# Kernel tuning notes

Hardware: AMD Instinct MI355X
Metric: run time of the kernel (lower is better)

The kernel has to match this reference:

```python
import jax, jax.numpy as jnp
import numpy as np

B, T, D = 32, 512, 384
DUR_MAX = 8                 # durations drawn in [0, DUR_MAX)
MAX_OUT = T * (DUR_MAX - 1) # static upper bound on total expanded length (3584)
ALPHA = 1.0


def setup_inputs() -> dict:
    key = jax.random.key(0)
    k1, k2 = jax.random.split(key)
    x = jax.random.normal(k1, (B, T, D), dtype=jnp.float32)
    durations = jax.random.randint(k2, (B, T), 0, DUR_MAX, dtype=jnp.int32)
    return {"input": x, "durations": durations}


def reference(input, durations):
    # patched_dur = clamp(round(alpha * dur), min=0)
    patched = jnp.round(ALPHA * durations.astype(jnp.float32)).astype(jnp.int32)
    patched = jnp.maximum(patched, 0)                       # [B, T]
    cum = jnp.cumsum(patched, axis=1)                       # [B, T] exclusive-right boundaries
    total = cum[:, -1:]                                      # [B, 1] true expanded lengths

    pos = jnp.arange(MAX_OUT, dtype=jnp.int32)               # [MAX_OUT]
    # output frame j comes from token idx = first t with cum[t] > j
    idx = jax.vmap(lambda c: jnp.searchsorted(c, pos, side='right'))(cum)  # [B, MAX_OUT]
    idx = jnp.clip(idx, 0, T - 1)
    valid = pos[None, :] < total                              # [B, MAX_OUT]

    out = jnp.take_along_axis(input, idx[:, :, None], axis=1)  # [B, MAX_OUT, D]
    return jnp.where(valid[:, :, None], out, jnp.zeros((), dtype=input.dtype))
```

## Files before the change

kernel.cpp:

```cpp
#include <hip/hip_runtime.h>

#define NB 32
#define NT 512
#define ND 384
#define DUR_MAX 8
#define MAX_OUT (NT * (DUR_MAX - 1))
#define NV (ND / 4)
#define NWG ((NB * MAX_OUT * NV) / 256)

__global__ __launch_bounds__(NT) void lr_scan_scatter(
    const int* __restrict__ dur, int* __restrict__ idxmap)
{
    __shared__ int wsum[NT / 64];
    const int b    = blockIdx.x;
    const int t    = threadIdx.x;
    const int lane = t & 63;
    const int w    = t >> 6;

    int d = dur[b * NT + t];
    d = d > 0 ? d : 0;

    int v = d;
    #pragma unroll
    for (int off = 1; off < 64; off <<= 1) {
        int u = __shfl_up(v, off);
        if (lane >= off) v += u;
    }
    if (lane == 63) wsum[w] = v;
    __syncthreads();
    if (t == 0) {
        int acc = 0;
        #pragma unroll
        for (int i = 0; i < NT / 64; ++i) { acc += wsum[i]; wsum[i] = acc; }
    }
    __syncthreads();
    const int cum   = v + (w ? wsum[w - 1] : 0);
    const int total = wsum[NT / 64 - 1];
    const int start = cum - d;

    int* base = idxmap + b * MAX_OUT;
    const int src = (b * NT + t) * NV;
    for (int j = 0; j < d; ++j) base[start + j] = src;
    for (int s = total + t; s < MAX_OUT; s += NT) base[s] = -1;
}

__global__ __launch_bounds__(256) void lr_gather(
    const float4* __restrict__ in, const int* __restrict__ idxmap,
    float4* __restrict__ out)
{
    const unsigned bid = blockIdx.x;
    const unsigned per = NWG / 8;
    const unsigned swz = (bid & 7u) * per + (bid >> 3);
    const unsigned g   = swz * 256u + threadIdx.x;
    const unsigned row = g / NV;
    const unsigned col = g - row * NV;

    const int src = idxmap[row];
    float4 r = make_float4(0.f, 0.f, 0.f, 0.f);
    if (src >= 0) r = in[src + col];
    out[g] = r;
}

extern "C" void kernel_launch(void* const* d_in, const int* in_sizes, int n_in,
                              void* d_out, int out_size, void* d_ws, size_t ws_size,
                              hipStream_t stream)
{
    const float* x   = (const float*)d_in[0];
    const int*   dur = (const int*)d_in[1];
    float* out = (float*)d_out;

    int* idxmap = (int*)d_ws;

    lr_scan_scatter<<<NB, NT, 0, stream>>>(dur, idxmap);
    lr_gather<<<NWG, 256, 0, stream>>>((const float4*)x, idxmap, (float4*)out);
}
```

Measured before the change: 197.9 us.

## Fuse duration scan and gather into one kernel with per-window shared index map

Replaces the separate scan/scatter and gather kernels with one fused kernel. Each block recomputes the per-batch prefix sum over durations and builds a shared-memory index map for one of 16 output windows, then gathers rows straight into the output. This drops the global idxmap round trip and the second launch. In exchange every block redoes the 512-element scan and adds a barrier, and padded positions now issue a dummy load from row 0.

```diff
diff --git a/kernel.cpp b/kernel.cpp
--- a/kernel.cpp
+++ b/kernel.cpp
@@ -6,16 +6,29 @@
 #define DUR_MAX 8
 #define MAX_OUT (NT * (DUR_MAX - 1))
 #define NV (ND / 4)
-#define NWG ((NB * MAX_OUT * NV) / 256)
+#define NWIN 16
+#define WPOS (MAX_OUT / NWIN)
+#define NBLK (NB * NWIN)
+#define VPT (WPOS * NV / NT)
 
-__global__ __launch_bounds__(NT) void lr_scan_scatter(
-    const int* __restrict__ dur, int* __restrict__ idxmap)
+__global__ __launch_bounds__(NT) void lr_fused(
+    const int* __restrict__ dur, const float4* __restrict__ in,
+    float4* __restrict__ out)
 {
     __shared__ int wsum[NT / 64];
-    const int b    = blockIdx.x;
+    __shared__ int ridx[WPOS];
+
+    const unsigned bid = blockIdx.x;
+    const unsigned l   = (bid & 7u) * (NBLK / 8u) + (bid >> 3);
+    const int b  = (int)(l >> 4);
+    const int wb = (int)(l & 15u);
+    const int p0 = wb * WPOS;
+
     const int t    = threadIdx.x;
     const int lane = t & 63;
     const int w    = t >> 6;
+
+    if (t < WPOS) ridx[t] = -1;
 
     int d = dur[b * NT + t];
     d = d > 0 ? d : 0;
@@ -35,30 +48,26 @@
     }
     __syncthreads();
     const int cum   = v + (w ? wsum[w - 1] : 0);
-    const int total = wsum[NT / 64 - 1];
     const int start = cum - d;
 
-    int* base = idxmap + b * MAX_OUT;
+    int lo = start - p0;        if (lo < 0) lo = 0;
+    int hi = start + d - p0;    if (hi > WPOS) hi = WPOS;
     const int src = (b * NT + t) * NV;
-    for (int j = 0; j < d; ++j) base[start + j] = src;
-    for (int s = total + t; s < MAX_OUT; s += NT) base[s] = -1;
-}
+    for (int j = lo; j < hi; ++j) ridx[j] = src;
+    __syncthreads();
 
-__global__ __launch_bounds__(256) void lr_gather(
-    const float4* __restrict__ in, const int* __restrict__ idxmap,
-    float4* __restrict__ out)
-{
-    const unsigned bid = blockIdx.x;
-    const unsigned per = NWG / 8;
-    const unsigned swz = (bid & 7u) * per + (bid >> 3);
-    const unsigned g   = swz * 256u + threadIdx.x;
-    const unsigned row = g / NV;
-    const unsigned col = g - row * NV;
-
-    const int src = idxmap[row];
-    float4 r = make_float4(0.f, 0.f, 0.f, 0.f);
-    if (src >= 0) r = in[src + col];
-    out[g] = r;
+    float4* ob = out + ((size_t)b * MAX_OUT + p0) * NV;
+    for (int i = 0; i < VPT; ++i) {
+        const int g = i * NT + t;
+        const int r = g / NV;
+        const int c = g - r * NV;
+        const int s = ridx[r];
+        const int sa = s >= 0 ? s : 0;
+        const float4 ld = in[sa + c];
+        float4 val = make_float4(0.f, 0.f, 0.f, 0.f);
+        if (s >= 0) val = ld;
+        ob[g] = val;
+    }
 }
 
 extern "C" void kernel_launch(void* const* d_in, const int* in_sizes, int n_in,
@@ -69,8 +78,5 @@
     const int*   dur = (const int*)d_in[1];
     float* out = (float*)d_out;
 
-    int* idxmap = (int*)d_ws;
-
-    lr_scan_scatter<<<NB, NT, 0, stream>>>(dur, idxmap);
-    lr_gather<<<NWG, 256, 0, stream>>>((const float4*)x, idxmap, (float4*)out);
+    lr_fused<<<NBLK, NT, 0, stream>>>(dur, (const float4*)x, (float4*)out);
 }
```

Measured after the change: 203.4 us. 1.03x slower.
